# Performance work log

Hardware: AMD Instinct MI355X
Metric: run time of the kernel (lower is better)

Reference implementation:

```python
import jax, jax.numpy as jnp
import numpy as np

B_, T_, D_, H_ = 16, 512, 256, 256
SCALE = 0.1


def setup_inputs() -> dict:
    key = jax.random.key(0)
    ks = jax.random.split(key, 4)
    s = 0.05  # xavier-ish init scale
    return {
        "x": jax.random.normal(ks[0], (B_, T_, D_), dtype=jnp.float32),
        "W_w": jax.random.normal(ks[1], (4 * H_, D_), dtype=jnp.float32) * s,
        "W_b": jnp.zeros((4 * H_,), dtype=jnp.float32),
        "U_w": jax.random.normal(ks[2], (4 * H_, H_), dtype=jnp.float32) * s,
        "U_b": jnp.zeros((4 * H_,), dtype=jnp.float32),
        "B_w": jax.random.normal(ks[3], (H_, D_, H_), dtype=jnp.float32) * s,
        "B_b": jnp.zeros((H_,), dtype=jnp.float32),
    }


def reference(x, W_w, W_b, U_w, U_b, B_w, B_b):
    # x: [B,T,D]; W_w: [4H,D]; U_w: [4H,H]; B_w: [H,D,H] (torch Bilinear layout)
    B, T, D = x.shape
    H = U_w.shape[1]
    # Precompute the input projection for all timesteps in one big GEMM
    Wx = jnp.einsum('btd,gd->btg', x, W_w) + W_b  # [B,T,4H]

    def step(carry, inp):
        h, c = carry
        wx_t, x_t = inp  # [B,4H], [B,D]
        gates = wx_t + h @ U_w.T + U_b
        i, f, o, g = jnp.split(gates, 4, axis=-1)
        i = jax.nn.sigmoid(i)
        f = jax.nn.sigmoid(f)
        o = jax.nn.sigmoid(o)
        g = jnp.tanh(g)
        # torch Bilinear: out[b,o] = sum_{d,h} x[b,d] W[o,d,h] h[b,h] + bias
        m = jnp.tanh(jnp.einsum('bd,odh,bh->bo', x_t, B_w, h) + B_b)
        c = f * c + i * g + SCALE * m
        h = o * jnp.tanh(c)
        return (h, c), h

    h0 = jnp.zeros((B, H), dtype=x.dtype)
    c0 = jnp.zeros((B, H), dtype=x.dtype)
    (h, c), outs = jax.lax.scan(
        step, (h0, c0), (jnp.swapaxes(Wx, 0, 1), jnp.swapaxes(x, 0, 1)))
    return jnp.swapaxes(outs, 0, 1), (h, c)  # ([B,T,H], ([B,H],[B,H]))
```

## Files before the change

kernel.cpp:

```cpp
#include <hip/hip_runtime.h>

typedef unsigned short u16;
typedef unsigned int u32;
typedef unsigned long long u64;
typedef short s16x8 __attribute__((ext_vector_type(8)));
typedef float f32x4 __attribute__((ext_vector_type(4)));
typedef __bf16 bf16x2 __attribute__((ext_vector_type(2)));

#define BTH 2097152

__device__ __forceinline__ u16 f2bf(float f) {
  u32 u = __float_as_uint(f);
  u32 r = (u + 0x7FFFu + ((u >> 16) & 1u)) >> 16;
  return (u16)r;
}
__device__ __forceinline__ float bf2f(u16 u) {
  return __uint_as_float(((u32)u) << 16);
}
__device__ __forceinline__ float sigm_(float x) { return 1.f / (1.f + __expf(-x)); }
__device__ __forceinline__ float tanh_(float x) {
  x = fminf(15.f, fmaxf(-15.f, x));
  float e = __expf(2.f * x);
  return (e - 1.f) / (e + 1.f);
}

#if defined(__has_builtin)
#if __has_builtin(__builtin_amdgcn_fdot2_f32_bf16)
#define HAVE_BF16_DOT2 1
#endif
#endif

__device__ __forceinline__ float dotp(u32 a, u32 b, float acc) {
#ifdef HAVE_BF16_DOT2
  return __builtin_amdgcn_fdot2_f32_bf16(__builtin_bit_cast(bf16x2, a),
                                         __builtin_bit_cast(bf16x2, b), acc, false);
#else
  acc += bf2f((u16)(a & 0xFFFFu)) * bf2f((u16)(b & 0xFFFFu));
  acc += bf2f((u16)(a >> 16)) * bf2f((u16)(b >> 16));
  return acc;
#endif
}

__device__ __forceinline__ void async_cp16(const u16* g, u16* l) {
  __builtin_amdgcn_global_load_lds(
      (const __attribute__((address_space(1))) void*)g,
      (__attribute__((address_space(3))) void*)l, 16, 0, 0);
}

__global__ void cast_x_kernel(const float* __restrict__ x, u16* __restrict__ xb) {
  int e = blockIdx.x * 256 + threadIdx.x;
  int d = e & 255;
  int r = e >> 8;
  int bb = r >> 9, t = r & 511;
  xb[(size_t)((t << 4) | bb) * 256 + d] = f2bf(x[e]);
}

__global__ void cast_w_kernel(const float* __restrict__ w, u16* __restrict__ o, int n) {
  int e = blockIdx.x * 256 + threadIdx.x;
  if (e < n) o[e] = f2bf(w[e]);
}

__global__ void transpose_b_kernel(const float* __restrict__ Bw, u16* __restrict__ Btt) {
  __shared__ float T[64][65];
  const int o = blockIdx.y;
  const int d0 = (blockIdx.x >> 2) * 64;
  const int h0 = (blockIdx.x & 3) * 64;
  const int tid = threadIdx.x;
  const float* src = Bw + (size_t)o * 65536;
#pragma unroll
  for (int k = 0; k < 16; ++k) {
    int idx = tid + k * 256;
    int rr = idx >> 6, cc = idx & 63;
    T[rr][cc] = src[(size_t)(d0 + rr) * 256 + h0 + cc];
  }
  __syncthreads();
#pragma unroll
  for (int k = 0; k < 16; ++k) {
    int idx = tid + k * 256;
    int rr = idx >> 6, cc = idx & 63;
    Btt[(size_t)(o * 256 + h0 + rr) * 256 + d0 + cc] = f2bf(T[cc][rr]);
  }
}

__global__ __launch_bounds__(256) void gemm_wx(
    const u16* __restrict__ A, const u16* __restrict__ Bm,
    float* __restrict__ Cf, int N,
    const float* __restrict__ bias0, const float* __restrict__ bias1) {
  __shared__ u16 As[128 * 32];
  __shared__ u16 Bs[128 * 32];
  const int tid = threadIdx.x;
  const int m0 = blockIdx.x * 128;
  const int n0 = blockIdx.y * 128;
  const int wave = tid >> 6, lane = tid & 63;
  const int wm = (wave >> 1) * 64, wn = (wave & 1) * 64;
  const int qm = lane & 15, quad = lane >> 4;
  f32x4 acc[4][4] = {};
  const int c0 = tid, c1 = tid + 256;
  const size_t ga0 = (size_t)(m0 + (c0 >> 2)) * 256 + (c0 & 3) * 8;
  const size_t ga1 = (size_t)(m0 + (c1 >> 2)) * 256 + (c1 & 3) * 8;
  const size_t gb0 = (size_t)(n0 + (c0 >> 2)) * 256 + (c0 & 3) * 8;
  const size_t gb1 = (size_t)(n0 + (c1 >> 2)) * 256 + (c1 & 3) * 8;

  for (int k0 = 0; k0 < 256; k0 += 32) {
    __syncthreads();
    async_cp16(A + ga0 + k0, As + c0 * 8);
    async_cp16(A + ga1 + k0, As + c1 * 8);
    async_cp16(Bm + gb0 + k0, Bs + c0 * 8);
    async_cp16(Bm + gb1 + k0, Bs + c1 * 8);
    __syncthreads();
    s16x8 af[4], bfr[4];
#pragma unroll
    for (int i = 0; i < 4; ++i)
      af[i] = *(const s16x8*)&As[(wm + i * 16 + qm) * 32 + quad * 8];
#pragma unroll
    for (int j = 0; j < 4; ++j)
      bfr[j] = *(const s16x8*)&Bs[(wn + j * 16 + qm) * 32 + quad * 8];
#pragma unroll
    for (int i = 0; i < 4; ++i)
#pragma unroll
      for (int j = 0; j < 4; ++j)
        acc[i][j] = __builtin_amdgcn_mfma_f32_16x16x32_bf16(af[i], bfr[j], acc[i][j], 0, 0, 0);
  }
#pragma unroll
  for (int i = 0; i < 4; ++i) {
    int rg = m0 + wm + i * 16 + quad * 4;
#pragma unroll
    for (int j = 0; j < 4; ++j) {
      int cg = n0 + wn + j * 16 + qm;
      float bias = bias0[cg] + bias1[cg];
#pragma unroll
      for (int r = 0; r < 4; ++r)
        Cf[(size_t)(rg + r) * (size_t)N + cg] = acc[i][j][r] + bias;
    }
  }
}

__global__ __launch_bounds__(512, 2) void fused_kernel(
    const u16* __restrict__ Ysc, const float* __restrict__ wx,
    const u16* __restrict__ Ubt, const float* __restrict__ Bb,
    float* cbuf, u64* hdata, float* __restrict__ out, int t0, int Tcur,
    const u16* __restrict__ Ag, const u16* __restrict__ Bg,
    u16* __restrict__ Ygm, int sblocks) {
  __shared__ __align__(16) char smem[24576];
  if ((int)blockIdx.x >= sblocks) {
    u16* As = (u16*)smem;
    u16* Bs = (u16*)(smem + 8192);
    const int gb = (int)blockIdx.x - sblocks;
    const int mt = gb >> 8, nt = gb & 255;
    const int tid = threadIdx.x;
    const int m0 = mt * 128, n0 = nt * 256;
    const int wave = tid >> 6, lane = tid & 63;
    const int wm = (wave >> 2) * 64, wn = (wave & 3) * 64;
    const int qm = lane & 15, quad = lane >> 4;
    f32x4 acc[4][4] = {};
    const size_t ga = (size_t)(m0 + (tid >> 2)) * 256 + (tid & 3) * 8;
    const int c0 = tid, c1 = tid + 512;
    const size_t gb0 = (size_t)(n0 + (c0 >> 2)) * 256 + (c0 & 3) * 8;
    const size_t gb1 = (size_t)(n0 + (c1 >> 2)) * 256 + (c1 & 3) * 8;
    for (int k0 = 0; k0 < 256; k0 += 32) {
      __syncthreads();
      async_cp16(Ag + ga + k0, As + tid * 8);
      async_cp16(Bg + gb0 + k0, Bs + c0 * 8);
      async_cp16(Bg + gb1 + k0, Bs + c1 * 8);
      __syncthreads();
      s16x8 af[4], bfr[4];
#pragma unroll
      for (int i = 0; i < 4; ++i)
        af[i] = *(const s16x8*)&As[(wm + i * 16 + qm) * 32 + quad * 8];
#pragma unroll
      for (int j = 0; j < 4; ++j)
        bfr[j] = *(const s16x8*)&Bs[(wn + j * 16 + qm) * 32 + quad * 8];
#pragma unroll
      for (int i = 0; i < 4; ++i)
#pragma unroll
        for (int j = 0; j < 4; ++j)
          acc[i][j] = __builtin_amdgcn_mfma_f32_16x16x32_bf16(af[i], bfr[j], acc[i][j], 0, 0, 0);
    }
#pragma unroll
    for (int i = 0; i < 4; ++i) {
      int rg = m0 + wm + i * 16 + quad * 4;
#pragma unroll
      for (int j = 0; j < 4; ++j) {
        int cg = n0 + wn + j * 16 + qm;
#pragma unroll
        for (int r = 0; r < 4; ++r)
          Ygm[(size_t)(rg + r) * 65536 + cg] = f2bf(acc[i][j][r]);
      }
    }
    return;
  }
  u32(*lh)[128] = (u32(*)[128])smem;
  int* lflag = (int*)(smem + 1024);
  const int tid = threadIdx.x;
  const int b = blockIdx.x >> 2;
  const int p = blockIdx.x & 3;
  const int oo = tid >> 3;
  const int s = tid & 7;
  const int o = (p << 6) + oo;
  const int wave = tid >> 6;
  const int lane = tid & 63;

  uint4 Ur[4][4];
  const uint4* Ub4 = (const uint4*)Ubt;
#pragma unroll
  for (int g = 0; g < 4; ++g) {
    int row = (g << 8) + o;
#pragma unroll
    for (int j = 0; j < 4; ++j) Ur[g][j] = Ub4[(size_t)row * 32 + s * 4 + j];
  }

  float c = cbuf[(b << 8) + o];
  const float bbias = Bb[o];
  if (tid < 2) lflag[tid] = t0 - 1;

  const int tend = t0 + Tcur;
  const u16* Yp = Ysc + (size_t)b * 65536 + (size_t)o * 256 + s * 32;
  uint4 Yc[4];
  {
    const uint4* y0 = (const uint4*)Yp;
    Yc[0] = y0[0]; Yc[1] = y0[1]; Yc[2] = y0[2]; Yc[3] = y0[3];
  }
  const float* wxp0 = wx + ((size_t)t0 * 16 + b) * 1024 + o;
  float w0 = wxp0[0], w1 = wxp0[256], w2 = wxp0[512], w3 = wxp0[768];
  float hn = 0.f;
  u64* hg = hdata + ((size_t)b << 8);
  __syncthreads();

  for (int t = t0; t < tend; ++t) {
    int dn = (t + 1 < tend) ? (t + 1 - t0) : (t - t0);
    const uint4* ynp = (const uint4*)(Yp + (size_t)dn * 1048576);
    uint4 yn0 = ynp[0], yn1 = ynp[1], yn2 = ynp[2], yn3 = ynp[3];
    int tn = (t + 1 < tend) ? (t + 1) : t;
    const float* nwp = wx + ((size_t)tn * 16 + b) * 1024 + o;
    float nw0 = nwp[0], nw1 = nwp[256], nw2 = nwp[512], nw3 = nwp[768];

    const int par = t & 1;
    if (wave == 0) {
      const u64* hp = hg + (par << 7) + (lane << 1);
      u64 v0, v1;
      for (;;) {
        v0 = __hip_atomic_load(hp, __ATOMIC_RELAXED, __HIP_MEMORY_SCOPE_AGENT);
        v1 = __hip_atomic_load(hp + 1, __ATOMIC_RELAXED, __HIP_MEMORY_SCOPE_AGENT);
        int ok = ((u32)(v0 >> 32) == (u32)t) & ((u32)(v1 >> 32) == (u32)t);
        if (__all(ok)) break;
      }
      lh[par][(lane << 1)] = (u32)v0;
      lh[par][(lane << 1) + 1] = (u32)v1;
      __hip_atomic_store(&lflag[par], t, __ATOMIC_RELEASE, __HIP_MEMORY_SCOPE_WORKGROUP);
    } else {
      while (__hip_atomic_load(&lflag[par], __ATOMIC_ACQUIRE, __HIP_MEMORY_SCOPE_WORKGROUP) < t) {}
    }

    uint4 hq[4];
    {
      const uint4* lp = (const uint4*)&lh[par][s << 4];
      hq[0] = lp[0]; hq[1] = lp[1]; hq[2] = lp[2]; hq[3] = lp[3];
    }

    float a0 = 0.f, a1 = 0.f, a2 = 0.f, a3 = 0.f, am = 0.f;
#pragma unroll
    for (int j = 0; j < 4; ++j) {
      u32 h0 = hq[j].x, h1 = hq[j].y, h2 = hq[j].z, h3 = hq[j].w;
      a0 = dotp(Ur[0][j].x, h0, a0); a0 = dotp(Ur[0][j].y, h1, a0);
      a0 = dotp(Ur[0][j].z, h2, a0); a0 = dotp(Ur[0][j].w, h3, a0);
      a1 = dotp(Ur[1][j].x, h0, a1); a1 = dotp(Ur[1][j].y, h1, a1);
      a1 = dotp(Ur[1][j].z, h2, a1); a1 = dotp(Ur[1][j].w, h3, a1);
      a2 = dotp(Ur[2][j].x, h0, a2); a2 = dotp(Ur[2][j].y, h1, a2);
      a2 = dotp(Ur[2][j].z, h2, a2); a2 = dotp(Ur[2][j].w, h3, a2);
      a3 = dotp(Ur[3][j].x, h0, a3); a3 = dotp(Ur[3][j].y, h1, a3);
      a3 = dotp(Ur[3][j].z, h2, a3); a3 = dotp(Ur[3][j].w, h3, a3);
      am = dotp(Yc[j].x, h0, am);   am = dotp(Yc[j].y, h1, am);
      am = dotp(Yc[j].z, h2, am);   am = dotp(Yc[j].w, h3, am);
    }
#pragma unroll
    for (int mk = 1; mk < 8; mk <<= 1) {
      a0 += __shfl_xor(a0, mk, 8);
      a1 += __shfl_xor(a1, mk, 8);
      a2 += __shfl_xor(a2, mk, 8);
      a3 += __shfl_xor(a3, mk, 8);
      am += __shfl_xor(am, mk, 8);
    }
    float gi = sigm_(a0 + w0);
    float gf = sigm_(a1 + w1);
    float go = sigm_(a2 + w2);
    float gg = tanh_(a3 + w3);
    float mm = tanh_(am + bbias);
    c = gf * c + gi * gg + 0.1f * mm;
    hn = go * tanh_(c);

    float hnext = __shfl_down(hn, 8);
    if (s == 0) {
      if (!(oo & 1)) {
        u32 pk = (u32)f2bf(hn) | ((u32)f2bf(hnext) << 16);
        u64 pk64 = ((u64)(u32)(t + 1) << 32) | (u64)pk;
        __hip_atomic_store(hg + (((size_t)((t + 1) & 1)) << 7) + (p << 5) + (oo >> 1),
                           pk64, __ATOMIC_RELAXED, __HIP_MEMORY_SCOPE_AGENT);
      }
      out[((size_t)b * 512 + t) * 256 + o] = hn;
    }
    Yc[0] = yn0; Yc[1] = yn1; Yc[2] = yn2; Yc[3] = yn3;
    w0 = nw0; w1 = nw1; w2 = nw2; w3 = nw3;
  }
  if (s == 0) {
    cbuf[(b << 8) + o] = c;
    out[(size_t)BTH + (b << 8) + o] = hn;
    out[(size_t)BTH + 4096 + (b << 8) + o] = c;
  }
}

extern "C" void kernel_launch(void* const* d_in, const int* in_sizes, int n_in,
                              void* d_out, int out_size, void* d_ws, size_t ws_size,
                              hipStream_t stream) {
  const float* x  = (const float*)d_in[0];
  const float* Ww = (const float*)d_in[1];
  const float* Wb = (const float*)d_in[2];
  const float* Uw = (const float*)d_in[3];
  const float* Ub = (const float*)d_in[4];
  const float* Bw = (const float*)d_in[5];
  const float* Bb = (const float*)d_in[6];
  float* out = (float*)d_out;

  char* ws = (char*)d_ws;
  const size_t WX_B  = (size_t)512 * 16 * 1024 * 4;
  const size_t XB_B  = (size_t)8192 * 256 * 2;
  const size_t BTT_B = (size_t)65536 * 256 * 2;
  const size_t WBT_B = (size_t)1024 * 256 * 2;
  const size_t UBT_B = (size_t)1024 * 256 * 2;
  const size_t CB_B  = 16384;
  const size_t HD_B  = 32768;
  const size_t ST_B  = CB_B + HD_B;
  const size_t fixedB = WX_B + XB_B + BTT_B + WBT_B + UBT_B + ST_B;
  size_t avail = (ws_size > fixedB) ? (ws_size - fixedB) : 0;
  long Tc = (long)(avail / (2 * 2097152));
  if (Tc > 64) Tc = 64;
  Tc &= ~7L;
  if (Tc < 8) Tc = 8;

  size_t YB   = (size_t)Tc * 2097152;
  u16* Y0     = (u16*)ws;
  u16* Y1     = (u16*)(ws + YB);
  float* wx   = (float*)(ws + 2 * YB);
  u16* xb     = (u16*)(ws + 2 * YB + WX_B);
  u16* Btt    = (u16*)(ws + 2 * YB + WX_B + XB_B);
  u16* Wbt    = (u16*)(ws + 2 * YB + WX_B + XB_B + BTT_B);
  u16* Ubt    = (u16*)(ws + 2 * YB + WX_B + XB_B + BTT_B + WBT_B);
  char* st    = ws + 2 * YB + WX_B + XB_B + BTT_B + WBT_B + UBT_B;
  float* cbuf = (float*)st;
  u64* hdata  = (u64*)(st + CB_B);

  hipMemsetAsync(st, 0, ST_B, stream);
  cast_x_kernel<<<8192, 256, 0, stream>>>(x, xb);
  cast_w_kernel<<<1024, 256, 0, stream>>>(Ww, Wbt, 262144);
  cast_w_kernel<<<1024, 256, 0, stream>>>(Uw, Ubt, 262144);
  transpose_b_kernel<<<dim3(16, 256), 256, 0, stream>>>(Bw, Btt);
  gemm_wx<<<dim3(64, 8), 256, 0, stream>>>(xb, Wbt, wx, 1024, Wb, Ub);

  {
    int Tc0 = (512 < Tc) ? 512 : (int)Tc;
    int ng = (Tc0 * 16 / 128) * 256;
    fused_kernel<<<ng, 512, 0, stream>>>(nullptr, wx, Ubt, Bb, cbuf, hdata, out,
                                         0, 0, xb, Btt, Y0, 0);
  }
  int cidx = 0;
  for (int t0 = 0; t0 < 512; t0 += (int)Tc, ++cidx) {
    int Tcur = (512 - t0 < (int)Tc) ? (512 - t0) : (int)Tc;
    int t0n = t0 + Tcur;
    u16* Ysc = (cidx & 1) ? Y1 : Y0;
    int ng = 0;
    const u16* Ag = xb;
    u16* Ygm = (cidx & 1) ? Y0 : Y1;
    if (t0n < 512) {
      int Tcn = (512 - t0n < (int)Tc) ? (512 - t0n) : (int)Tc;
      ng = (Tcn * 16 / 128) * 256;
      Ag = xb + (size_t)t0n * 4096;
    }
    fused_kernel<<<64 + ng, 512, 0, stream>>>(Ysc, wx, Ubt, Bb, cbuf, hdata, out,
                                              t0, Tcur, Ag, Btt, Ygm, 64);
  }
}
```

Baseline: 1.364 ms.

## Merge prep kernels into one launch and fold Wx GEMM into fused kernel

Replaces the memset, the x/W/U cast kernels and the B transpose with a single prep_kernel that branches on block index, and zeroes the state buffer inside it. The standalone Wx projection GEMM is removed and its tiles run as extra blocks in the first fused_kernel launch, next to the first chunk's bilinear Y GEMM. This cuts kernel launches and gaps between them, at the cost of more branching and a larger first fused launch.

```diff
diff --git a/kernel.cpp b/kernel.cpp
--- a/kernel.cpp
+++ b/kernel.cpp
@@ -47,91 +47,47 @@
       (__attribute__((address_space(3))) void*)l, 16, 0, 0);
 }
 
-__global__ void cast_x_kernel(const float* __restrict__ x, u16* __restrict__ xb) {
-  int e = blockIdx.x * 256 + threadIdx.x;
-  int d = e & 255;
-  int r = e >> 8;
-  int bb = r >> 9, t = r & 511;
-  xb[(size_t)((t << 4) | bb) * 256 + d] = f2bf(x[e]);
-}
-
-__global__ void cast_w_kernel(const float* __restrict__ w, u16* __restrict__ o, int n) {
-  int e = blockIdx.x * 256 + threadIdx.x;
-  if (e < n) o[e] = f2bf(w[e]);
-}
-
-__global__ void transpose_b_kernel(const float* __restrict__ Bw, u16* __restrict__ Btt) {
-  __shared__ float T[64][65];
-  const int o = blockIdx.y;
-  const int d0 = (blockIdx.x >> 2) * 64;
-  const int h0 = (blockIdx.x & 3) * 64;
+__global__ __launch_bounds__(256) void prep_kernel(
+    const float* __restrict__ x, const float* __restrict__ Ww,
+    const float* __restrict__ Uw, const float* __restrict__ Bw,
+    u16* __restrict__ xb, u16* __restrict__ Wbt, u16* __restrict__ Ubt,
+    u16* __restrict__ Btt, u64* __restrict__ stz) {
+  const int bid = blockIdx.x;
   const int tid = threadIdx.x;
-  const float* src = Bw + (size_t)o * 65536;
-#pragma unroll
-  for (int k = 0; k < 16; ++k) {
-    int idx = tid + k * 256;
-    int rr = idx >> 6, cc = idx & 63;
-    T[rr][cc] = src[(size_t)(d0 + rr) * 256 + h0 + cc];
-  }
-  __syncthreads();
-#pragma unroll
-  for (int k = 0; k < 16; ++k) {
-    int idx = tid + k * 256;
-    int rr = idx >> 6, cc = idx & 63;
-    Btt[(size_t)(o * 256 + h0 + rr) * 256 + d0 + cc] = f2bf(T[cc][rr]);
-  }
-}
-
-__global__ __launch_bounds__(256) void gemm_wx(
-    const u16* __restrict__ A, const u16* __restrict__ Bm,
-    float* __restrict__ Cf, int N,
-    const float* __restrict__ bias0, const float* __restrict__ bias1) {
-  __shared__ u16 As[128 * 32];
-  __shared__ u16 Bs[128 * 32];
-  const int tid = threadIdx.x;
-  const int m0 = blockIdx.x * 128;
-  const int n0 = blockIdx.y * 128;
-  const int wave = tid >> 6, lane = tid & 63;
-  const int wm = (wave >> 1) * 64, wn = (wave & 1) * 64;
-  const int qm = lane & 15, quad = lane >> 4;
-  f32x4 acc[4][4] = {};
-  const int c0 = tid, c1 = tid + 256;
-  const size_t ga0 = (size_t)(m0 + (c0 >> 2)) * 256 + (c0 & 3) * 8;
-  const size_t ga1 = (size_t)(m0 + (c1 >> 2)) * 256 + (c1 & 3) * 8;
-  const size_t gb0 = (size_t)(n0 + (c0 >> 2)) * 256 + (c0 & 3) * 8;
-  const size_t gb1 = (size_t)(n0 + (c1 >> 2)) * 256 + (c1 & 3) * 8;
-
-  for (int k0 = 0; k0 < 256; k0 += 32) {
+  if (bid < 8192) {
+    int e = bid * 256 + tid;
+    int d = e & 255;
+    int r = e >> 8;
+    int bb = r >> 9, t = r & 511;
+    xb[(size_t)((t << 4) | bb) * 256 + d] = f2bf(x[e]);
+  } else if (bid < 9216) {
+    int e = (bid - 8192) * 256 + tid;
+    Wbt[e] = f2bf(Ww[e]);
+  } else if (bid < 10240) {
+    int e = (bid - 9216) * 256 + tid;
+    Ubt[e] = f2bf(Uw[e]);
+  } else if (bid < 14336) {
+    __shared__ float T[64][65];
+    int tb = bid - 10240;
+    int o = tb >> 4, xi = tb & 15;
+    const int d0 = (xi >> 2) * 64;
+    const int h0 = (xi & 3) * 64;
+    const float* src = Bw + (size_t)o * 65536;
+#pragma unroll
+    for (int k = 0; k < 16; ++k) {
+      int idx = tid + k * 256;
+      int rr = idx >> 6, cc = idx & 63;
+      T[rr][cc] = src[(size_t)(d0 + rr) * 256 + h0 + cc];
+    }
     __syncthreads();
-    async_cp16(A + ga0 + k0, As + c0 * 8);
-    async_cp16(A + ga1 + k0, As + c1 * 8);
-    async_cp16(Bm + gb0 + k0, Bs + c0 * 8);
-    async_cp16(Bm + gb1 + k0, Bs + c1 * 8);
-    __syncthreads();
-    s16x8 af[4], bfr[4];
-#pragma unroll
-    for (int i = 0; i < 4; ++i)
-      af[i] = *(const s16x8*)&As[(wm + i * 16 + qm) * 32 + quad * 8];
-#pragma unroll
-    for (int j = 0; j < 4; ++j)
-      bfr[j] = *(const s16x8*)&Bs[(wn + j * 16 + qm) * 32 + quad * 8];
-#pragma unroll
-    for (int i = 0; i < 4; ++i)
-#pragma unroll
-      for (int j = 0; j < 4; ++j)
-        acc[i][j] = __builtin_amdgcn_mfma_f32_16x16x32_bf16(af[i], bfr[j], acc[i][j], 0, 0, 0);
-  }
-#pragma unroll
-  for (int i = 0; i < 4; ++i) {
-    int rg = m0 + wm + i * 16 + quad * 4;
-#pragma unroll
-    for (int j = 0; j < 4; ++j) {
-      int cg = n0 + wn + j * 16 + qm;
-      float bias = bias0[cg] + bias1[cg];
-#pragma unroll
-      for (int r = 0; r < 4; ++r)
-        Cf[(size_t)(rg + r) * (size_t)N + cg] = acc[i][j][r] + bias;
-    }
+#pragma unroll
+    for (int k = 0; k < 16; ++k) {
+      int idx = tid + k * 256;
+      int rr = idx >> 6, cc = idx & 63;
+      Btt[(size_t)(o * 256 + h0 + rr) * 256 + d0 + cc] = f2bf(T[cc][rr]);
+    }
+  } else {
+    for (int i = tid; i < 6144; i += 256) stz[i] = 0ull;
   }
 }
 
@@ -140,28 +96,43 @@
     const u16* __restrict__ Ubt, const float* __restrict__ Bb,
     float* cbuf, u64* hdata, float* __restrict__ out, int t0, int Tcur,
     const u16* __restrict__ Ag, const u16* __restrict__ Bg,
-    u16* __restrict__ Ygm, int sblocks) {
+    u16* __restrict__ Ygm,
+    const u16* __restrict__ Wbt, const float* __restrict__ Wb,
+    const float* __restrict__ Ub, float* __restrict__ wxout,
+    int sblocks, int wxblocks) {
   __shared__ __align__(16) char smem[24576];
+  const int tid = threadIdx.x;
   if ((int)blockIdx.x >= sblocks) {
     u16* As = (u16*)smem;
     u16* Bs = (u16*)(smem + 8192);
-    const int gb = (int)blockIdx.x - sblocks;
-    const int mt = gb >> 8, nt = gb & 255;
-    const int tid = threadIdx.x;
-    const int m0 = mt * 128, n0 = nt * 256;
+    const int gi = (int)blockIdx.x - sblocks;
+    const bool iswx = gi < wxblocks;
+    int mt, n0;
+    const u16* Bop;
+    if (iswx) {
+      mt = gi >> 2;
+      n0 = (gi & 3) * 256;
+      Bop = Wbt;
+    } else {
+      int g2 = gi - wxblocks;
+      mt = g2 >> 8;
+      n0 = (g2 & 255) * 256;
+      Bop = Bg;
+    }
+    const u16* A = Ag + (size_t)mt * 128 * 256;
     const int wave = tid >> 6, lane = tid & 63;
     const int wm = (wave >> 2) * 64, wn = (wave & 3) * 64;
     const int qm = lane & 15, quad = lane >> 4;
     f32x4 acc[4][4] = {};
-    const size_t ga = (size_t)(m0 + (tid >> 2)) * 256 + (tid & 3) * 8;
+    const size_t ga = (size_t)(tid >> 2) * 256 + (tid & 3) * 8;
     const int c0 = tid, c1 = tid + 512;
     const size_t gb0 = (size_t)(n0 + (c0 >> 2)) * 256 + (c0 & 3) * 8;
     const size_t gb1 = (size_t)(n0 + (c1 >> 2)) * 256 + (c1 & 3) * 8;
     for (int k0 = 0; k0 < 256; k0 += 32) {
       __syncthreads();
-      async_cp16(Ag + ga + k0, As + tid * 8);
-      async_cp16(Bg + gb0 + k0, Bs + c0 * 8);
-      async_cp16(Bg + gb1 + k0, Bs + c1 * 8);
+      async_cp16(A + ga + k0, As + tid * 8);
+      async_cp16(Bop + gb0 + k0, Bs + c0 * 8);
+      async_cp16(Bop + gb1 + k0, Bs + c1 * 8);
       __syncthreads();
       s16x8 af[4], bfr[4];
 #pragma unroll
@@ -176,22 +147,36 @@
         for (int j = 0; j < 4; ++j)
           acc[i][j] = __builtin_amdgcn_mfma_f32_16x16x32_bf16(af[i], bfr[j], acc[i][j], 0, 0, 0);
     }
-#pragma unroll
-    for (int i = 0; i < 4; ++i) {
-      int rg = m0 + wm + i * 16 + quad * 4;
-#pragma unroll
-      for (int j = 0; j < 4; ++j) {
-        int cg = n0 + wn + j * 16 + qm;
-#pragma unroll
-        for (int r = 0; r < 4; ++r)
-          Ygm[(size_t)(rg + r) * 65536 + cg] = f2bf(acc[i][j][r]);
+    if (iswx) {
+#pragma unroll
+      for (int i = 0; i < 4; ++i) {
+        int rg = mt * 128 + wm + i * 16 + quad * 4;
+#pragma unroll
+        for (int j = 0; j < 4; ++j) {
+          int cg = n0 + wn + j * 16 + qm;
+          float bias = Wb[cg] + Ub[cg];
+#pragma unroll
+          for (int r = 0; r < 4; ++r)
+            wxout[(size_t)(rg + r) * 1024 + cg] = acc[i][j][r] + bias;
+        }
+      }
+    } else {
+#pragma unroll
+      for (int i = 0; i < 4; ++i) {
+        int rg = wm + i * 16 + quad * 4;
+#pragma unroll
+        for (int j = 0; j < 4; ++j) {
+          int cg = n0 + wn + j * 16 + qm;
+#pragma unroll
+          for (int r = 0; r < 4; ++r)
+            Ygm[(size_t)(mt * 128 + rg + r) * 65536 + cg] = f2bf(acc[i][j][r]);
+        }
       }
     }
     return;
   }
   u32(*lh)[128] = (u32(*)[128])smem;
   int* lflag = (int*)(smem + 1024);
-  const int tid = threadIdx.x;
   const int b = blockIdx.x >> 2;
   const int p = blockIdx.x & 3;
   const int oo = tid >> 3;
@@ -348,33 +333,30 @@
   float* cbuf = (float*)st;
   u64* hdata  = (u64*)(st + CB_B);
 
-  hipMemsetAsync(st, 0, ST_B, stream);
-  cast_x_kernel<<<8192, 256, 0, stream>>>(x, xb);
-  cast_w_kernel<<<1024, 256, 0, stream>>>(Ww, Wbt, 262144);
-  cast_w_kernel<<<1024, 256, 0, stream>>>(Uw, Ubt, 262144);
-  transpose_b_kernel<<<dim3(16, 256), 256, 0, stream>>>(Bw, Btt);
-  gemm_wx<<<dim3(64, 8), 256, 0, stream>>>(xb, Wbt, wx, 1024, Wb, Ub);
+  prep_kernel<<<14337, 256, 0, stream>>>(x, Ww, Uw, Bw, xb, Wbt, Ubt, Btt, (u64*)st);
 
   {
-    int Tc0 = (512 < Tc) ? 512 : (int)Tc;
-    int ng = (Tc0 * 16 / 128) * 256;
-    fused_kernel<<<ng, 512, 0, stream>>>(nullptr, wx, Ubt, Bb, cbuf, hdata, out,
-                                         0, 0, xb, Btt, Y0, 0);
+    int Tc0 = (int)Tc;
+    int ng0 = (Tc0 * 16 / 128) * 256;
+    fused_kernel<<<256 + ng0, 512, 0, stream>>>(
+        nullptr, wx, Ubt, Bb, cbuf, hdata, out, 0, 0,
+        xb, Btt, Y0, Wbt, Wb, Ub, wx, 0, 256);
   }
   int cidx = 0;
   for (int t0 = 0; t0 < 512; t0 += (int)Tc, ++cidx) {
     int Tcur = (512 - t0 < (int)Tc) ? (512 - t0) : (int)Tc;
     int t0n = t0 + Tcur;
     u16* Ysc = (cidx & 1) ? Y1 : Y0;
+    u16* Ygm = (cidx & 1) ? Y0 : Y1;
     int ng = 0;
     const u16* Ag = xb;
-    u16* Ygm = (cidx & 1) ? Y0 : Y1;
     if (t0n < 512) {
       int Tcn = (512 - t0n < (int)Tc) ? (512 - t0n) : (int)Tc;
       ng = (Tcn * 16 / 128) * 256;
       Ag = xb + (size_t)t0n * 4096;
     }
-    fused_kernel<<<64 + ng, 512, 0, stream>>>(Ysc, wx, Ubt, Bb, cbuf, hdata, out,
-                                              t0, Tcur, Ag, Btt, Ygm, 64);
-  }
-}
+    fused_kernel<<<64 + ng, 512, 0, stream>>>(
+        Ysc, wx, Ubt, Bb, cbuf, hdata, out, t0, Tcur,
+        Ag, Btt, Ygm, Wbt, Wb, Ub, wx, 64, 0);
+  }
+}
```

Measured after the change: 1.356 ms. About the same (-0.6%).
